# Optimization experiments

Hardware: AMD Instinct MI355X
Metric: run time of the kernel (lower is better)

## Reference

```python
import jax, jax.numpy as jnp
import numpy as np

NUM_USERS = 1024
NUM_BUSINESSES = 2048
N_NODES = NUM_USERS + NUM_BUSINESSES  # 3072
B = 1024            # batch size (== NUM_USERS to keep the business_idx-offset bug valid)
E = 16384           # edges (self loops added inside reference, PyG GATConv default)
H = 768             # hidden_size
HEADS = 8
NUM_IMAGES = 3


def setup_inputs() -> dict:
    key = jax.random.key(0)
    ks = jax.random.split(key, 24)
    def rn(k, shape, s=0.02):
        return jax.random.normal(k, shape, dtype=jnp.float32) * s
    inp = {
        'text_cls': rn(ks[0], (B, 768), 1.0),              # BERT CLS features
        'img_cls': rn(ks[1], (B, NUM_IMAGES, 768), 1.0),   # ViT CLS features per image
        'biz_feats': rn(ks[2], (B, 3), 1.0),
        'W_text': rn(ks[3], (768, H)), 'b_text': jnp.zeros((H,), jnp.float32),
        'W_img': rn(ks[4], (768, H)), 'b_img': jnp.zeros((H,), jnp.float32),
        'W_bf': rn(ks[5], (3, H)), 'b_bf': jnp.zeros((H,), jnp.float32),
        'user_table': rn(ks[6], (NUM_USERS, H)),
        'biz_table': rn(ks[7], (NUM_BUSINESSES, H)),
        'W1': rn(ks[8], (H, HEADS * H)),
        'att_src1': rn(ks[9], (HEADS, H), 0.1),
        'att_dst1': rn(ks[10], (HEADS, H), 0.1),
        'b1': jnp.zeros((HEADS * H,), jnp.float32),
        'W2': rn(ks[11], (HEADS * H, H)),
        'att_src2': rn(ks[12], (1, H), 0.1),
        'att_dst2': rn(ks[13], (1, H), 0.1),
        'b2': jnp.zeros((H,), jnp.float32),
        'Wf1': rn(ks[14], (4 * H, 2 * H)), 'bf1': jnp.zeros((2 * H,), jnp.float32),
        'Wf2': rn(ks[15], (2 * H, H)), 'bf2': jnp.zeros((H,), jnp.float32),
        'Wf3': rn(ks[16], (H, 1)), 'bf3': jnp.zeros((1,), jnp.float32),
        'user_idx': jax.random.randint(ks[17], (B,), 0, NUM_USERS),
        'business_idx': jax.random.randint(ks[18], (B,), NUM_USERS, N_NODES),
        'edge_index': jax.random.randint(ks[19], (2, E), 0, N_NODES),
    }
    return inp


def gat_conv(x, src, dst, W, a_src, a_dst, bias, heads):
    # PyG GATConv: linear -> per-head additive attention -> scatter softmax over dst -> scatter add
    N = x.shape[0]
    C = W.shape[1] // heads
    h = (x @ W).reshape(N, heads, C)                       # [N,H,C]
    s_src = jnp.sum(h * a_src, axis=-1)                    # [N,H]
    s_dst = jnp.sum(h * a_dst, axis=-1)                    # [N,H]
    e = jax.nn.leaky_relu(s_src[src] + s_dst[dst], 0.2)    # [E,H]
    e_max = jax.ops.segment_max(e, dst, num_segments=N)    # [N,H]
    ee = jnp.exp(e - e_max[dst])
    denom = jax.ops.segment_sum(ee, dst, num_segments=N)   # [N,H]
    alpha = ee / (denom[dst] + 1e-16)                      # [E,H]
    out = jax.ops.segment_sum(h[src] * alpha[..., None], dst, num_segments=N)  # [N,H,C]
    return out.reshape(N, heads * C) + bias


def reference(text_cls, img_cls, biz_feats, W_text, b_text, W_img, b_img, W_bf, b_bf,
              user_table, biz_table, W1, att_src1, att_dst1, b1, W2, att_src2, att_dst2, b2,
              Wf1, bf1, Wf2, bf2, Wf3, bf3, user_idx, business_idx, edge_index):
    text_emb = text_cls @ W_text + b_text                       # TextEncoder.fc
    img_emb = jnp.mean(img_cls, axis=1) @ W_img + b_img         # ImageEncoder mean + fc
    meta = biz_feats @ W_bf + b_bf                              # business_feature_fc
    user_emb = user_table[user_idx]
    biz_emb = biz_table[business_idx - user_idx.shape[0]]       # faithful: offset by batch size
    x = jnp.zeros((N_NODES, H), jnp.float32)
    x = x.at[user_idx].set(user_emb)
    x = x.at[business_idx].set((text_emb + img_emb + meta + biz_emb) / 4.0)
    loop = jnp.arange(N_NODES)
    src = jnp.concatenate([edge_index[0], loop])                # add self loops (PyG default)
    dst = jnp.concatenate([edge_index[1], loop])
    x = jax.nn.relu(gat_conv(x, src, dst, W1, att_src1, att_dst1, b1, HEADS))
    x = gat_conv(x, src, dst, W2, att_src2, att_dst2, b2, 1)
    cat = jnp.concatenate([x[user_idx], x[business_idx], text_emb, img_emb], axis=1)  # [B,4H]
    h1 = jax.nn.relu(cat @ Wf1 + bf1)
    h2 = jax.nn.relu(h1 @ Wf2 + bf2)
    return (h2 @ Wf3 + bf3).squeeze(-1)                         # [B]
```

## Files before the change

kernel.cpp:

```cpp
#include <hip/hip_runtime.h>
#include <hip/hip_bf16.h>

namespace {

constexpr int kB = 1024;
constexpr int kNU = 1024;
constexpr int kNB = 2048;
constexpr int kNN = 3072;
constexpr int kE = 16384;
constexpr int kET = kE + kNN;
constexpr int kH = 768;
constexpr int kHeads = 8;
constexpr int kS2 = 8;

typedef __attribute__((ext_vector_type(8))) short bf16x8_t;
typedef __attribute__((ext_vector_type(4))) float f32x4_t;

__device__ __forceinline__ float tof(float x) { return x; }
__device__ __forceinline__ float tof(__hip_bfloat16 x) { return __bfloat162float(x); }
__device__ __forceinline__ void stor(float* p, float v) { *p = v; }
__device__ __forceinline__ void stor(__hip_bfloat16* p, float v) { *p = __float2bfloat16(v); }

__device__ __forceinline__ float blo(unsigned u) {
  union { unsigned u; float f; } c; c.u = u << 16; return c.f;
}
__device__ __forceinline__ float bhi(unsigned u) {
  union { unsigned u; float f; } c; c.u = u & 0xffff0000u; return c.f;
}

__device__ __forceinline__ unsigned pk2(float a, float b) {
  union { __hip_bfloat16 h[2]; unsigned u; } c;
  c.h[0] = __float2bfloat16(a); c.h[1] = __float2bfloat16(b);
  return c.u;
}

__device__ __forceinline__ void gload_lds16(const void* g, void* l) {
  __builtin_amdgcn_global_load_lds(
      (const __attribute__((address_space(1))) void*)g,
      (__attribute__((address_space(3))) void*)l, 16, 0, 0);
}

template <int G>
__device__ __forceinline__ void wait_stage(bool more) {
  if (more) {
    if constexpr (G == 2) asm volatile("s_waitcnt vmcnt(2)" ::: "memory");
    else if constexpr (G == 3) asm volatile("s_waitcnt vmcnt(3)" ::: "memory");
    else asm volatile("s_waitcnt vmcnt(4)" ::: "memory");
  } else {
    asm volatile("s_waitcnt vmcnt(0)" ::: "memory");
  }
  __builtin_amdgcn_sched_barrier(0);
  asm volatile("s_barrier" ::: "memory");
  __builtin_amdgcn_sched_barrier(0);
}

template <int BM, int BN, int FM, int FN, typename TC>
__device__ __forceinline__ void gemm_body(
    const __hip_bfloat16* __restrict__ A, const __hip_bfloat16* __restrict__ Bt,
    const float* __restrict__ bias, TC* __restrict__ C,
    int K, int lda, int ldc, int act, int bx, int by) {
  __shared__ __align__(16) __hip_bfloat16 As[3][BM][32];
  __shared__ __align__(16) __hip_bfloat16 Bs[3][BN][32];
  constexpr int G = BM / 64 + BN / 64;
  const int t = threadIdx.x;
  const int w = t >> 6, lane = t & 63;
  const int wm = w >> 1, wn = w & 1;
  const int bm = by * BM, bn = bx * BN;
  const int lr = lane & 15, lg = lane >> 4;

  f32x4_t acc[FM][FN];
#pragma unroll
  for (int m = 0; m < FM; ++m)
#pragma unroll
    for (int n = 0; n < FN; ++n) acc[m][n] = (f32x4_t){0.f, 0.f, 0.f, 0.f};

  auto stage = [&](int buf, int kt) {
    const int k0 = kt << 5;
#pragma unroll
    for (int i = 0; i < BM / 64; ++i) {
      int L = i * 256 + t;
      gload_lds16(A + (size_t)(bm + (L >> 2)) * lda + k0 + (L & 3) * 8,
                  (char*)(&As[buf][0][0]) + ((size_t)(i * 256 + w * 64)) * 16);
    }
#pragma unroll
    for (int i = 0; i < BN / 64; ++i) {
      int L = i * 256 + t;
      gload_lds16(Bt + (size_t)(bn + (L >> 2)) * K + k0 + (L & 3) * 8,
                  (char*)(&Bs[buf][0][0]) + ((size_t)(i * 256 + w * 64)) * 16);
    }
  };

  const int NT = K >> 5;
  stage(0, 0);
  if (NT > 1) stage(1, 1);
  int cur = 0;
  for (int kt = 0; kt < NT; ++kt) {
    wait_stage<G>(kt + 1 < NT);
    if (kt + 2 < NT) {
      int sb = cur + 2; if (sb >= 3) sb -= 3;
      stage(sb, kt + 2);
    }
    bf16x8_t af[FM], bv[FN];
#pragma unroll
    for (int m = 0; m < FM; ++m)
      af[m] = *(const bf16x8_t*)&As[cur][wm * FM * 16 + m * 16 + lr][lg * 8];
#pragma unroll
    for (int n = 0; n < FN; ++n)
      bv[n] = *(const bf16x8_t*)&Bs[cur][wn * FN * 16 + n * 16 + lr][lg * 8];
#pragma unroll
    for (int m = 0; m < FM; ++m)
#pragma unroll
      for (int n = 0; n < FN; ++n)
        acc[m][n] = __builtin_amdgcn_mfma_f32_16x16x32_bf16(af[m], bv[n], acc[m][n], 0, 0, 0);
    cur = (cur == 2) ? 0 : cur + 1;
  }

#pragma unroll
  for (int m = 0; m < FM; ++m) {
    const int row0 = bm + wm * FM * 16 + m * 16 + lg * 4;
#pragma unroll
    for (int n = 0; n < FN; ++n) {
      const int cn = bn + wn * FN * 16 + n * 16 + lr;
      const float bvv = bias ? bias[cn] : 0.f;
#pragma unroll
      for (int r = 0; r < 4; ++r) {
        float v = acc[m][n][r] + bvv;
        if (act) v = fmaxf(v, 0.f);
        stor(&C[(size_t)(row0 + r) * ldc + cn], v);
      }
    }
  }
}

__device__ __forceinline__ void swz_xy(bool mfast, int& bx, int& by) {
  const int nwg = gridDim.x * gridDim.y;
  const int orig = blockIdx.y * gridDim.x + blockIdx.x;
  const int swz = (orig & 7) * (nwg >> 3) + (orig >> 3);
  if (mfast) { by = swz % gridDim.y; bx = swz / gridDim.y; }
  else       { bx = swz % gridDim.x; by = swz / gridDim.x; }
}

template <int BM, int BN, int FM, int FN>
__global__ __launch_bounds__(256) void mfma_gemm_dual(
    const __hip_bfloat16* __restrict__ A0, const __hip_bfloat16* __restrict__ Bt0,
    const float* __restrict__ bias0, float* __restrict__ C0,
    const __hip_bfloat16* __restrict__ A1, const __hip_bfloat16* __restrict__ Bt1,
    const float* __restrict__ bias1, float* __restrict__ C1,
    int N, int K) {
  int bx, by;
  swz_xy(true, bx, by);
  const __hip_bfloat16* A = blockIdx.z ? A1 : A0;
  const __hip_bfloat16* Bt = blockIdx.z ? Bt1 : Bt0;
  const float* bias = blockIdx.z ? bias1 : bias0;
  float* C = blockIdx.z ? C1 : C0;
  gemm_body<BM, BN, FM, FN, float>(A, Bt, bias, C, K, K, N, 0, bx, by);
}

template <int BM, int BN, int FM, int FN>
__global__ __launch_bounds__(256) void gemm_head(
    const __hip_bfloat16* __restrict__ y, const __hip_bfloat16* __restrict__ W1t,
    const float* __restrict__ b1, __hip_bfloat16* __restrict__ x2) {
  const int hd = blockIdx.x;
  const int tile = blockIdx.y;
  const int bx = tile % (kH / BN);
  const int by = tile / (kH / BN);
  gemm_body<BM, BN, FM, FN, __hip_bfloat16>(
      y + (size_t)hd * kH, W1t + (size_t)hd * kH * kH, b1 + hd * kH,
      x2 + (size_t)hd * kH, kH, kHeads * kH, kHeads * kH, 1, bx, by);
}

template <int BM, int BN, int FM, int FN, int S>
__global__ __launch_bounds__(256) void mfma_gemm_kpin(
    const __hip_bfloat16* __restrict__ A, const __hip_bfloat16* __restrict__ Bt,
    float* __restrict__ Cpart, int M, int N, int K) {
  __shared__ __align__(16) __hip_bfloat16 As[3][BM][32];
  __shared__ __align__(16) __hip_bfloat16 Bs[3][BN][32];
  constexpr int G = BM / 64 + BN / 64;
  const int kc = blockIdx.x;
  const int tile = blockIdx.y;
  const int tilesN = N / BN;
  const int bx = tile % tilesN;
  const int by = tile / tilesN;
  const int KC = K / S;
  const int kbeg = kc * KC;
  const int t = threadIdx.x;
  const int w = t >> 6, lane = t & 63;
  const int wm = w >> 1, wn = w & 1;
  const int bm = by * BM, bn = bx * BN;
  const int lr = lane & 15, lg = lane >> 4;

  f32x4_t acc[FM][FN];
#pragma unroll
  for (int m = 0; m < FM; ++m)
#pragma unroll
    for (int n = 0; n < FN; ++n) acc[m][n] = (f32x4_t){0.f, 0.f, 0.f, 0.f};

  auto stage = [&](int buf, int kt) {
    const int k0 = kbeg + (kt << 5);
#pragma unroll
    for (int i = 0; i < BM / 64; ++i) {
      int L = i * 256 + t;
      gload_lds16(A + (size_t)(bm + (L >> 2)) * K + k0 + (L & 3) * 8,
                  (char*)(&As[buf][0][0]) + ((size_t)(i * 256 + w * 64)) * 16);
    }
#pragma unroll
    for (int i = 0; i < BN / 64; ++i) {
      int L = i * 256 + t;
      gload_lds16(Bt + (size_t)(bn + (L >> 2)) * K + k0 + (L & 3) * 8,
                  (char*)(&Bs[buf][0][0]) + ((size_t)(i * 256 + w * 64)) * 16);
    }
  };

  const int NT = KC >> 5;
  stage(0, 0);
  if (NT > 1) stage(1, 1);
  int cur = 0;
  for (int kt = 0; kt < NT; ++kt) {
    wait_stage<G>(kt + 1 < NT);
    if (kt + 2 < NT) {
      int sb = cur + 2; if (sb >= 3) sb -= 3;
      stage(sb, kt + 2);
    }
    bf16x8_t af[FM], bv[FN];
#pragma unroll
    for (int m = 0; m < FM; ++m)
      af[m] = *(const bf16x8_t*)&As[cur][wm * FM * 16 + m * 16 + lr][lg * 8];
#pragma unroll
    for (int n = 0; n < FN; ++n)
      bv[n] = *(const bf16x8_t*)&Bs[cur][wn * FN * 16 + n * 16 + lr][lg * 8];
#pragma unroll
    for (int m = 0; m < FM; ++m)
#pragma unroll
      for (int n = 0; n < FN; ++n)
        acc[m][n] = __builtin_amdgcn_mfma_f32_16x16x32_bf16(af[m], bv[n], acc[m][n], 0, 0, 0);
    cur = (cur == 2) ? 0 : cur + 1;
  }

  float* Cp = Cpart + (size_t)kc * M * N;
#pragma unroll
  for (int m = 0; m < FM; ++m) {
    const int row0 = bm + wm * FM * 16 + m * 16 + lg * 4;
#pragma unroll
    for (int n = 0; n < FN; ++n) {
      const int cn = bn + wn * FN * 16 + n * 16 + lr;
#pragma unroll
      for (int r = 0; r < 4; ++r) Cp[(size_t)(row0 + r) * N + cn] = acc[m][n][r];
    }
  }
}

template <int BM, int BN, int FM, int FN>
__global__ __launch_bounds__(256) void mfma_gemm_splitk(
    const __hip_bfloat16* __restrict__ A, const __hip_bfloat16* __restrict__ Bt,
    float* __restrict__ Cpart, int M, int N, int K, int KC) {
  __shared__ __align__(16) __hip_bfloat16 As[3][BM][32];
  __shared__ __align__(16) __hip_bfloat16 Bs[3][BN][32];
  constexpr int G = BM / 64 + BN / 64;
  int bx, by;
  swz_xy(false, bx, by);
  const int t = threadIdx.x;
  const int w = t >> 6, lane = t & 63;
  const int wm = w >> 1, wn = w & 1;
  const int bm = by * BM, bn = bx * BN;
  const int kbeg = blockIdx.z * KC;
  const int lr = lane & 15, lg = lane >> 4;

  f32x4_t acc[FM][FN];
#pragma unroll
  for (int m = 0; m < FM; ++m)
#pragma unroll
    for (int n = 0; n < FN; ++n) acc[m][n] = (f32x4_t){0.f, 0.f, 0.f, 0.f};

  auto stage = [&](int buf, int kt) {
    const int k0 = kbeg + (kt << 5);
#pragma unroll
    for (int i = 0; i < BM / 64; ++i) {
      int L = i * 256 + t;
      gload_lds16(A + (size_t)(bm + (L >> 2)) * K + k0 + (L & 3) * 8,
                  (char*)(&As[buf][0][0]) + ((size_t)(i * 256 + w * 64)) * 16);
    }
#pragma unroll
    for (int i = 0; i < BN / 64; ++i) {
      int L = i * 256 + t;
      gload_lds16(Bt + (size_t)(bn + (L >> 2)) * K + k0 + (L & 3) * 8,
                  (char*)(&Bs[buf][0][0]) + ((size_t)(i * 256 + w * 64)) * 16);
    }
  };

  const int NT = KC >> 5;
  stage(0, 0);
  if (NT > 1) stage(1, 1);
  int cur = 0;
  for (int kt = 0; kt < NT; ++kt) {
    wait_stage<G>(kt + 1 < NT);
    if (kt + 2 < NT) {
      int sb = cur + 2; if (sb >= 3) sb -= 3;
      stage(sb, kt + 2);
    }
    bf16x8_t af[FM], bv[FN];
#pragma unroll
    for (int m = 0; m < FM; ++m)
      af[m] = *(const bf16x8_t*)&As[cur][wm * FM * 16 + m * 16 + lr][lg * 8];
#pragma unroll
    for (int n = 0; n < FN; ++n)
      bv[n] = *(const bf16x8_t*)&Bs[cur][wn * FN * 16 + n * 16 + lr][lg * 8];
#pragma unroll
    for (int m = 0; m < FM; ++m)
#pragma unroll
      for (int n = 0; n < FN; ++n)
        acc[m][n] = __builtin_amdgcn_mfma_f32_16x16x32_bf16(af[m], bv[n], acc[m][n], 0, 0, 0);
    cur = (cur == 2) ? 0 : cur + 1;
  }

  float* Cp = Cpart + (size_t)blockIdx.z * M * N;
#pragma unroll
  for (int m = 0; m < FM; ++m) {
    const int row0 = bm + wm * FM * 16 + m * 16 + lg * 4;
#pragma unroll
    for (int n = 0; n < FN; ++n) {
      const int cn = bn + wn * FN * 16 + n * 16 + lr;
#pragma unroll
      for (int r = 0; r < 4; ++r) Cp[(size_t)(row0 + r) * N + cn] = acc[m][n][r];
    }
  }
}

__global__ __launch_bounds__(192) void reduce_scores2_kernel(
    const float* __restrict__ part, const float* __restrict__ att_src,
    const float* __restrict__ att_dst, __hip_bfloat16* __restrict__ h2,
    float* __restrict__ s_src, float* __restrict__ s_dst) {
  __shared__ float redS[3], redD[3];
  const int row = blockIdx.x;
  const int t = threadIdx.x;
  const int c = t * 4;
  const float* p = part + (size_t)row * kH + c;
  float4 s = *(const float4*)p;
#pragma unroll
  for (int z = 1; z < kS2; ++z) {
    float4 qv = *(const float4*)(p + (size_t)z * kNN * kH);
    s.x += qv.x; s.y += qv.y; s.z += qv.z; s.w += qv.w;
  }
  __hip_bfloat16 b0 = __float2bfloat16(s.x), b1 = __float2bfloat16(s.y);
  __hip_bfloat16 b2 = __float2bfloat16(s.z), b3 = __float2bfloat16(s.w);
  __hip_bfloat16* o = h2 + (size_t)row * kH + c;
  o[0] = b0; o[1] = b1; o[2] = b2; o[3] = b3;
  float f0 = tof(b0), f1 = tof(b1), f2 = tof(b2), f3 = tof(b3);
  float ss = f0 * att_src[c] + f1 * att_src[c + 1] + f2 * att_src[c + 2] + f3 * att_src[c + 3];
  float sd = f0 * att_dst[c] + f1 * att_dst[c + 1] + f2 * att_dst[c + 2] + f3 * att_dst[c + 3];
#pragma unroll
  for (int off = 32; off; off >>= 1) { ss += __shfl_down(ss, off); sd += __shfl_down(sd, off); }
  if ((t & 63) == 0) { redS[t >> 6] = ss; redD[t >> 6] = sd; }
  __syncthreads();
  if (t == 0) {
    s_src[row] = redS[0] + redS[1] + redS[2];
    s_dst[row] = redD[0] + redD[1] + redD[2];
  }
}

__global__ void reduce_relu_kernel(const float* __restrict__ part,
                                   const float* __restrict__ bias,
                                   __hip_bfloat16* __restrict__ outb, int MN4, int N) {
  int i = blockIdx.x * 256 + threadIdx.x;
  if (i >= MN4) return;
  float4 s = ((const float4*)part)[i];
  float4 p = ((const float4*)part)[(size_t)MN4 + i];
  int c = (i * 4) % N;
  float v0 = fmaxf(s.x + p.x + bias[c], 0.f);
  float v1 = fmaxf(s.y + p.y + bias[c + 1], 0.f);
  float v2 = fmaxf(s.z + p.z + bias[c + 2], 0.f);
  float v3 = fmaxf(s.w + p.w + bias[c + 3], 0.f);
  uint2 o;
  o.x = pk2(v0, v1); o.y = pk2(v2, v3);
  *(uint2*)(outb + (size_t)i * 4) = o;
}

__global__ __launch_bounds__(192) void reduce_final_kernel(
    const float* __restrict__ part, const float* __restrict__ bias,
    const float* __restrict__ Wf3, const float* __restrict__ bf3,
    float* __restrict__ out) {
  __shared__ float red[3];
  const int row = blockIdx.x;
  const int t = threadIdx.x;
  const int c = t * 4;
  const float* p0 = part + (size_t)row * kH + c;
  const float* p1 = p0 + (size_t)kB * kH;
  float4 a = *(const float4*)p0;
  float4 b = *(const float4*)p1;
  float v0 = fmaxf(a.x + b.x + bias[c], 0.f);
  float v1 = fmaxf(a.y + b.y + bias[c + 1], 0.f);
  float v2 = fmaxf(a.z + b.z + bias[c + 2], 0.f);
  float v3 = fmaxf(a.w + b.w + bias[c + 3], 0.f);
  float s = v0 * Wf3[c] + v1 * Wf3[c + 1] + v2 * Wf3[c + 2] + v3 * Wf3[c + 3];
#pragma unroll
  for (int off = 32; off; off >>= 1) s += __shfl_down(s, off);
  if ((t & 63) == 0) red[t >> 6] = s;
  __syncthreads();
  if (t == 0) out[row] = red[0] + red[1] + red[2] + bf3[0];
}

struct TJobs {
  const float* in[6];
  __hip_bfloat16* out[6];
  int K[6];
  int N[6];
  int start[7];
};

__global__ __launch_bounds__(256) void transp_prep_kernel(
    TJobs j, const float* __restrict__ text_cls, const float* __restrict__ img_cls,
    __hip_bfloat16* __restrict__ text_bf, __hip_bfloat16* __restrict__ imgm_bf,
    int prep_blocks, const float* __restrict__ W1, const float* __restrict__ a_src,
    const float* __restrict__ a_dst, float* __restrict__ wa,
    int wa_blocks, uint4* __restrict__ xb4) {
  __shared__ float tl[32][33];
  const int bid = blockIdx.x;
  const int t = threadIdx.x;
  if (bid >= j.start[6] + prep_blocks + wa_blocks) {
    int i = (bid - j.start[6] - prep_blocks - wa_blocks) * 256 + t;
    if (i < kNN * kH * 2 / 16) xb4[i] = (uint4){0u, 0u, 0u, 0u};
    return;
  }
  if (bid >= j.start[6] + prep_blocks) {
    int gw = ((bid - j.start[6] - prep_blocks) * 256 + t) >> 6;
    int lane = t & 63;
    if (gw >= kHeads * kH) return;
    int i = gw >> 3, hd = gw & 7;
    const float* wrow = W1 + (size_t)i * (kHeads * kH) + hd * kH;
    const float* as = a_src + (size_t)hd * kH;
    const float* ad = a_dst + (size_t)hd * kH;
    float ss = 0.f, sd = 0.f;
    for (int c = lane; c < kH; c += 64) {
      float wv = wrow[c];
      ss = fmaf(wv, as[c], ss);
      sd = fmaf(wv, ad[c], sd);
    }
#pragma unroll
    for (int o = 32; o; o >>= 1) { ss += __shfl_down(ss, o); sd += __shfl_down(sd, o); }
    if (lane == 0) {
      wa[hd * kH + i] = ss;
      wa[kHeads * kH + hd * kH + i] = sd;
    }
    return;
  }
  if (bid >= j.start[6]) {
    int idx = (bid - j.start[6]) * 256 + t;
    if (idx < kB * kH) {
      text_bf[idx] = __float2bfloat16(text_cls[idx]);
      int b = idx / kH, c = idx - b * kH;
      const float* p = img_cls + (size_t)b * 3 * kH + c;
      imgm_bf[idx] = __float2bfloat16((p[0] + p[kH] + p[2 * kH]) * (1.f / 3.f));
    }
    return;
  }
  int idx = 0;
#pragma unroll
  for (int q = 1; q < 6; ++q)
    if (bid >= j.start[q]) idx = q;
  const int tile = bid - j.start[idx];
  const int N = j.N[idx], K = j.K[idx];
  const int tilesN = N >> 5;
  const int n0 = (tile % tilesN) << 5, k0 = (tile / tilesN) << 5;
  const float* in = j.in[idx];
  __hip_bfloat16* out = j.out[idx];
  const int r = t >> 3, c = (t & 7) * 4;
#pragma unroll
  for (int i = 0; i < 4; ++i) tl[r][c + i] = in[(size_t)(k0 + r) * N + n0 + c + i];
  __syncthreads();
  __hip_bfloat16* op = out + (size_t)(n0 + r) * K + k0 + c;
#pragma unroll
  for (int i = 0; i < 4; ++i) op[i] = __float2bfloat16(tl[c + i][r]);
}

__global__ __launch_bounds__(256) void s1_kernel(const __hip_bfloat16* __restrict__ xb,
                                                 const float* __restrict__ wa,
                                                 float* __restrict__ s1s,
                                                 float* __restrict__ s1d) {
  __shared__ unsigned xrow[kH / 2];
  const int n = blockIdx.x;
  const int t = threadIdx.x;
  const unsigned* xp = (const unsigned*)(xb + (size_t)n * kH);
  if (t < 128) { xrow[t] = xp[t]; xrow[t + 128] = xp[t + 128]; xrow[t + 256] = xp[t + 256]; }
  __syncthreads();
  const int w = t >> 6, lane = t & 63;
  const float* ws0 = wa + (size_t)w * kH;
  const float* wd0 = wa + (size_t)(kHeads + w) * kH;
  const float* ws1 = wa + (size_t)(w + 4) * kH;
  const float* wd1 = wa + (size_t)(kHeads + w + 4) * kH;
  float s0 = 0.f, d0 = 0.f, s1 = 0.f, d1 = 0.f;
  for (int u = lane; u < kH / 2; u += 64) {
    unsigned v = xrow[u];
    float f0 = blo(v), f1 = bhi(v);
    int c = u * 2;
    s0 = fmaf(f0, ws0[c], fmaf(f1, ws0[c + 1], s0));
    d0 = fmaf(f0, wd0[c], fmaf(f1, wd0[c + 1], d0));
    s1 = fmaf(f0, ws1[c], fmaf(f1, ws1[c + 1], s1));
    d1 = fmaf(f0, wd1[c], fmaf(f1, wd1[c + 1], d1));
  }
#pragma unroll
  for (int o = 32; o; o >>= 1) {
    s0 += __shfl_down(s0, o); d0 += __shfl_down(d0, o);
    s1 += __shfl_down(s1, o); d1 += __shfl_down(d1, o);
  }
  if (lane == 0) {
    s1s[n * 8 + w] = s0;     s1d[n * 8 + w] = d0;
    s1s[n * 8 + w + 4] = s1; s1d[n * 8 + w + 4] = d1;
  }
}

__global__ __launch_bounds__(256) void agg1x_kernel(
    const int* __restrict__ rowptr, const int* __restrict__ cols,
    const float* __restrict__ s1s, const float* __restrict__ s1d,
    const __hip_bfloat16* __restrict__ xb, __hip_bfloat16* __restrict__ y) {
  __shared__ float mh[8], rdh[8], sdl[8];
  __shared__ float alph[128][9];
  const int n = blockIdx.x;
  const int t = threadIdx.x, w = t >> 6, lane = t & 63;
  const int beg = rowptr[n], end = rowptr[n + 1];
  if (t < 8) sdl[t] = s1d[n * 8 + t];
  __syncthreads();
#pragma unroll
  for (int p = 0; p < 2; ++p) {
    const int h = w + p * 4;
    const float sd = sdl[h];
    float m = -3.402823466e38f;
    for (int i = beg + lane; i < end; i += 64) {
      float e = s1s[(size_t)cols[i] * 8 + h] + sd;
      e = (e > 0.f) ? e : 0.2f * e;
      m = fmaxf(m, e);
    }
#pragma unroll
    for (int o = 32; o; o >>= 1) m = fmaxf(m, __shfl_xor(m, o));
    float ds = 0.f;
    for (int i = beg + lane; i < end; i += 64) {
      float e = s1s[(size_t)cols[i] * 8 + h] + sd;
      e = (e > 0.f) ? e : 0.2f * e;
      ds += expf(e - m);
    }
#pragma unroll
    for (int o = 32; o; o >>= 1) ds += __shfl_xor(ds, o);
    if (lane == 0) { mh[h] = m; rdh[h] = 1.f / (ds + 1e-16f); }
  }
  __syncthreads();

  float acc[8][4];
#pragma unroll
  for (int h = 0; h < 8; ++h)
#pragma unroll
    for (int q = 0; q < 4; ++q) acc[h][q] = 0.f;
  const int c0 = t * 4;

  for (int chunk = beg; chunk < end; chunk += 128) {
    const int cnt = min(128, end - chunk);
#pragma unroll
    for (int p = 0; p < 2; ++p) {
      const int h = w + p * 4;
      const float sd = sdl[h], m = mh[h], rd = rdh[h];
      for (int i = lane; i < cnt; i += 64) {
        float e = s1s[(size_t)cols[chunk + i] * 8 + h] + sd;
        e = (e > 0.f) ? e : 0.2f * e;
        alph[i][h] = expf(e - m) * rd;
      }
    }
    __syncthreads();
    if (t < 192) {
      for (int i = 0; i < cnt; ++i) {
        int src = cols[chunk + i];
        uint2 v = *(const uint2*)(xb + (size_t)src * kH + c0);
        float f0 = blo(v.x), f1 = bhi(v.x), f2 = blo(v.y), f3 = bhi(v.y);
#pragma unroll
        for (int h = 0; h < 8; ++h) {
          float a = alph[i][h];
          acc[h][0] = fmaf(a, f0, acc[h][0]);
          acc[h][1] = fmaf(a, f1, acc[h][1]);
          acc[h][2] = fmaf(a, f2, acc[h][2]);
          acc[h][3] = fmaf(a, f3, acc[h][3]);
        }
      }
    }
    __syncthreads();
  }
  if (t < 192) {
#pragma unroll
    for (int h = 0; h < 8; ++h) {
      uint2 o;
      o.x = pk2(acc[h][0], acc[h][1]);
      o.y = pk2(acc[h][2], acc[h][3]);
      *(uint2*)(y + ((size_t)n * 8 + h) * kH + c0) = o;
    }
  }
}

__global__ __launch_bounds__(1024) void scan_kernel(const int* __restrict__ ei,
                                                    int* __restrict__ rowptr,
                                                    int* __restrict__ cursor) {
  __shared__ int sdeg[kNN];
  __shared__ int sums[1024];
  int t = threadIdx.x;
#pragma unroll
  for (int i = 0; i < 3; ++i) sdeg[t * 3 + i] = 0;
  __syncthreads();
  for (int e = t; e < kET; e += 1024) {
    int dst = (e < kE) ? ei[kE + e] : (e - kE);
    atomicAdd(&sdeg[dst], 1);
  }
  __syncthreads();
  int v0 = sdeg[t * 3], v1 = sdeg[t * 3 + 1], v2 = sdeg[t * 3 + 2];
  int s = v0 + v1 + v2;
  sums[t] = s;
  __syncthreads();
  for (int o = 1; o < 1024; o <<= 1) {
    int xv = (t >= o) ? sums[t - o] : 0;
    __syncthreads();
    sums[t] += xv;
    __syncthreads();
  }
  int excl = sums[t] - s;
  rowptr[t * 3] = excl;          cursor[t * 3] = excl;
  rowptr[t * 3 + 1] = excl + v0; cursor[t * 3 + 1] = excl + v0;
  rowptr[t * 3 + 2] = excl + v0 + v1; cursor[t * 3 + 2] = excl + v0 + v1;
  if (t == 1023) rowptr[kNN] = excl + s;
}

constexpr int kFillBlocks = (kET + 255) / 256;

__global__ __launch_bounds__(256) void fill_build_kernel(
    const int* __restrict__ ei, int* __restrict__ cursor, int* __restrict__ cols,
    const int* __restrict__ user_idx, const float* __restrict__ user_table,
    const int* __restrict__ business_idx, const float* __restrict__ text_emb,
    const float* __restrict__ img_emb, const float* __restrict__ biz_feats,
    const float* __restrict__ W_bf, const float* __restrict__ b_bf,
    const float* __restrict__ biz_table, __hip_bfloat16* __restrict__ xb) {
  const int bid = blockIdx.x;
  if (bid < kFillBlocks) {
    int e = bid * 256 + threadIdx.x;
    if (e >= kET) return;
    int src, dst;
    if (e < kE) { src = ei[e]; dst = ei[kE + e]; } else { src = dst = e - kE; }
    int pos = atomicAdd(&cursor[dst], 1);
    cols[pos] = src;
    return;
  }
  const int b = bid - kFillBlocks;
  if (b < kNU) {
    int node = user_idx[b];
    for (int c = threadIdx.x; c < kH; c += 256)
      xb[(size_t)node * kH + c] = __float2bfloat16(user_table[(size_t)node * kH + c]);
  } else {
    const int m = b - kNU;
    int cand = -1;
    for (int i = threadIdx.x; i < kB; i += 256)
      if (business_idx[i] == kNU + m) cand = i;
#pragma unroll
    for (int o = 32; o; o >>= 1) cand = max(cand, __shfl_xor(cand, o));
    __shared__ int red[4];
    if ((threadIdx.x & 63) == 0) red[threadIdx.x >> 6] = cand;
    __syncthreads();
    const int w = max(max(red[0], red[1]), max(red[2], red[3]));
    if (w < 0) return;
    int node = kNU + m;
    float f0 = biz_feats[w * 3], f1 = biz_feats[w * 3 + 1], f2 = biz_feats[w * 3 + 2];
    for (int c = threadIdx.x; c < kH; c += 256) {
      float meta = f0 * W_bf[c] + f1 * W_bf[kH + c] + f2 * W_bf[2 * kH + c] + b_bf[c];
      float v = (text_emb[(size_t)w * kH + c] + img_emb[(size_t)w * kH + c] + meta +
                 biz_table[(size_t)m * kH + c]) * 0.25f;
      xb[(size_t)node * kH + c] = __float2bfloat16(v);
    }
  }
}

__global__ __launch_bounds__(256) void gat_agg_kernel(
    const int* __restrict__ rowptr, const int* __restrict__ cols,
    const float* __restrict__ s_src, const float* __restrict__ s_dst,
    const __hip_bfloat16* __restrict__ h, const float* __restrict__ bias,
    float* __restrict__ out_f, int total) {
  const int pair = blockIdx.x * 4 + (threadIdx.x >> 6);
  if (pair >= total) return;
  const int lane = threadIdx.x & 63;
  const int n = pair;
  const int beg = rowptr[n], end = rowptr[n + 1];
  const float sdv = s_dst[pair];

  float m = -3.402823466e38f;
  for (int i = beg + lane; i < end; i += 64) {
    float e = s_src[cols[i]] + sdv;
    e = (e > 0.f) ? e : 0.2f * e;
    m = fmaxf(m, e);
  }
#pragma unroll
  for (int o = 32; o; o >>= 1) m = fmaxf(m, __shfl_xor(m, o));

  float dsum = 0.f;
  for (int i = beg + lane; i < end; i += 64) {
    float e = s_src[cols[i]] + sdv;
    e = (e > 0.f) ? e : 0.2f * e;
    dsum += expf(e - m);
  }
#pragma unroll
  for (int o = 32; o; o >>= 1) dsum += __shfl_xor(dsum, o);
  const float rdsum = 1.f / (dsum + 1e-16f);

  float a[12];
#pragma unroll
  for (int q = 0; q < 12; ++q) a[q] = 0.f;
  const size_t hoff = (size_t)lane * 4;
  for (int i = beg; i < end; ++i) {
    int src = cols[i];
    float e = s_src[src] + sdv;
    e = (e > 0.f) ? e : 0.2f * e;
    float wgt = expf(e - m) * rdsum;
    const __hip_bfloat16* hp = h + (size_t)src * kH + hoff;
#pragma unroll
    for (int j = 0; j < 3; ++j) {
      uint2 v = *(const uint2*)(hp + j * 256);
      a[j * 4 + 0] = fmaf(wgt, blo(v.x), a[j * 4 + 0]);
      a[j * 4 + 1] = fmaf(wgt, bhi(v.x), a[j * 4 + 1]);
      a[j * 4 + 2] = fmaf(wgt, blo(v.y), a[j * 4 + 2]);
      a[j * 4 + 3] = fmaf(wgt, bhi(v.y), a[j * 4 + 3]);
    }
  }
  const size_t ob = (size_t)n * kH + hoff;
#pragma unroll
  for (int j = 0; j < 3; ++j) {
#pragma unroll
    for (int q = 0; q < 4; ++q)
      out_f[ob + j * 256 + q] = a[j * 4 + q] + bias[hoff + j * 256 + q];
  }
}

__global__ void cat_kernel(const float* __restrict__ xf, const float* __restrict__ text_emb,
                           const float* __restrict__ img_emb, const int* __restrict__ user_idx,
                           const int* __restrict__ business_idx, __hip_bfloat16* __restrict__ cat) {
  int b = blockIdx.x;
  int u = user_idx[b], z = business_idx[b];
  __hip_bfloat16* crow = cat + (size_t)b * 4 * kH;
  for (int c = threadIdx.x; c < kH; c += blockDim.x) {
    crow[c] = __float2bfloat16(xf[(size_t)u * kH + c]);
    crow[kH + c] = __float2bfloat16(xf[(size_t)z * kH + c]);
    crow[2 * kH + c] = __float2bfloat16(text_emb[(size_t)b * kH + c]);
    crow[3 * kH + c] = __float2bfloat16(img_emb[(size_t)b * kH + c]);
  }
}

}

extern "C" void kernel_launch(void* const* d_in, const int* in_sizes, int n_in,
                              void* d_out, int out_size, void* d_ws, size_t ws_size,
                              hipStream_t stream) {
  const float* text_cls = (const float*)d_in[0];
  const float* img_cls = (const float*)d_in[1];
  const float* biz_feats = (const float*)d_in[2];
  const float* W_text = (const float*)d_in[3];
  const float* b_text = (const float*)d_in[4];
  const float* W_img = (const float*)d_in[5];
  const float* b_img = (const float*)d_in[6];
  const float* W_bf = (const float*)d_in[7];
  const float* b_bf = (const float*)d_in[8];
  const float* user_table = (const float*)d_in[9];
  const float* biz_table = (const float*)d_in[10];
  const float* W1 = (const float*)d_in[11];
  const float* att_src1 = (const float*)d_in[12];
  const float* att_dst1 = (const float*)d_in[13];
  const float* b1 = (const float*)d_in[14];
  const float* W2 = (const float*)d_in[15];
  const float* att_src2 = (const float*)d_in[16];
  const float* att_dst2 = (const float*)d_in[17];
  const float* b2 = (const float*)d_in[18];
  const float* Wf1 = (const float*)d_in[19];
  const float* bf1 = (const float*)d_in[20];
  const float* Wf2 = (const float*)d_in[21];
  const float* bf2 = (const float*)d_in[22];
  const float* Wf3 = (const float*)d_in[23];
  const float* bf3 = (const float*)d_in[24];
  const int* user_idx = (const int*)d_in[25];
  const int* business_idx = (const int*)d_in[26];
  const int* edge_index = (const int*)d_in[27];
  float* out = (float*)d_out;
  (void)in_sizes; (void)n_in; (void)out_size; (void)ws_size;

  char* base = (char*)d_ws;
  size_t off = 0;
  auto alloc = [&](size_t bytes) -> void* {
    void* p = base + off;
    off = (off + bytes + 255) & ~(size_t)255;
    return p;
  };
  __hip_bfloat16* xb = (__hip_bfloat16*)alloc((size_t)kNN * kH * 2);
  __hip_bfloat16* text_bf = (__hip_bfloat16*)alloc((size_t)kB * kH * 2);
  __hip_bfloat16* imgm_bf = (__hip_bfloat16*)alloc((size_t)kB * kH * 2);
  float* text_emb = (float*)alloc((size_t)kB * kH * 4);
  float* img_emb = (float*)alloc((size_t)kB * kH * 4);
  __hip_bfloat16* Wtt = (__hip_bfloat16*)alloc((size_t)kH * kH * 2);
  __hip_bfloat16* Wit = (__hip_bfloat16*)alloc((size_t)kH * kH * 2);
  __hip_bfloat16* W1t = (__hip_bfloat16*)alloc((size_t)kHeads * kH * kH * 2);
  __hip_bfloat16* W2t = (__hip_bfloat16*)alloc((size_t)kH * kHeads * kH * 2);
  __hip_bfloat16* Wf1t = (__hip_bfloat16*)alloc((size_t)2 * kH * 4 * kH * 2);
  __hip_bfloat16* Wf2t = (__hip_bfloat16*)alloc((size_t)kH * 2 * kH * 2);
  float* wa = (float*)alloc((size_t)2 * kHeads * kH * 4);
  __hip_bfloat16* y = (__hip_bfloat16*)alloc((size_t)kNN * kHeads * kH * 2);
  char* ext = (char*)alloc((size_t)kNN * kHeads * kH * 2);
  float* part = (float*)y;
  float* xf = (float*)ext;
  __hip_bfloat16* catb = (__hip_bfloat16*)(ext + 9437184);
  __hip_bfloat16* m1 = (__hip_bfloat16*)(ext + 9437184 + 6291456);
  __hip_bfloat16* x2 = (__hip_bfloat16*)alloc((size_t)kNN * kHeads * kH * 2);
  __hip_bfloat16* h2 = (__hip_bfloat16*)alloc((size_t)kNN * kH * 2);
  float* s1s = (float*)alloc((size_t)kNN * kHeads * 4);
  float* s1d = (float*)alloc((size_t)kNN * kHeads * 4);
  float* s2s = (float*)alloc((size_t)kNN * 4);
  float* s2d = (float*)alloc((size_t)kNN * 4);
  int* rowptr = (int*)alloc((size_t)(kNN + 1) * 4);
  int* cursor = (int*)alloc((size_t)kNN * 4);
  int* cols = (int*)alloc((size_t)kET * 4);

  TJobs tj;
  tj.in[0] = W_text; tj.out[0] = Wtt;  tj.K[0] = kH;          tj.N[0] = kH;
  tj.in[1] = W_img;  tj.out[1] = Wit;  tj.K[1] = kH;          tj.N[1] = kH;
  tj.in[2] = W1;     tj.out[2] = W1t;  tj.K[2] = kH;          tj.N[2] = kHeads * kH;
  tj.in[3] = W2;     tj.out[3] = W2t;  tj.K[3] = kHeads * kH; tj.N[3] = kH;
  tj.in[4] = Wf1;    tj.out[4] = Wf1t; tj.K[4] = 4 * kH;      tj.N[4] = 2 * kH;
  tj.in[5] = Wf2;    tj.out[5] = Wf2t; tj.K[5] = 2 * kH;      tj.N[5] = kH;
  tj.start[0] = 0;
  for (int q = 0; q < 6; ++q)
    tj.start[q + 1] = tj.start[q] + (tj.K[q] / 32) * (tj.N[q] / 32);
  const int prep_blocks = (kB * kH + 255) / 256;
  const int wa_blocks = (kHeads * kH) / 4;
  const int init_blocks = (kNN * kH * 2 / 16 + 255) / 256;
  transp_prep_kernel<<<tj.start[6] + prep_blocks + wa_blocks + init_blocks, 256, 0, stream>>>(
      tj, text_cls, img_cls, text_bf, imgm_bf, prep_blocks, W1, att_src1, att_dst1, wa,
      wa_blocks, (uint4*)xb);

  mfma_gemm_dual<64, 128, 2, 4><<<dim3(kH / 128, kB / 64, 2), 256, 0, stream>>>(
      text_bf, Wtt, b_text, text_emb, imgm_bf, Wit, b_img, img_emb, kH, kH);

  scan_kernel<<<1, 1024, 0, stream>>>(edge_index, rowptr, cursor);
  fill_build_kernel<<<kFillBlocks + kNN, 256, 0, stream>>>(
      edge_index, cursor, cols, user_idx, user_table, business_idx, text_emb, img_emb,
      biz_feats, W_bf, b_bf, biz_table, xb);

  s1_kernel<<<kNN, 256, 0, stream>>>(xb, wa, s1s, s1d);
  agg1x_kernel<<<kNN, 256, 0, stream>>>(rowptr, cols, s1s, s1d, xb, y);
  gemm_head<128, 128, 4, 4><<<dim3(kHeads, (kNN / 128) * (kH / 128)), 256, 0, stream>>>(
      y, W1t, b1, x2);

  mfma_gemm_kpin<128, 128, 4, 4, kS2>
      <<<dim3(kS2, (kNN / 128) * (kH / 128)), 256, 0, stream>>>(
          x2, W2t, part, kNN, kH, kHeads * kH);
  reduce_scores2_kernel<<<kNN, 192, 0, stream>>>(part, att_src2, att_dst2, h2, s2s, s2d);
  gat_agg_kernel<<<kNN / 4, 256, 0, stream>>>(rowptr, cols, s2s, s2d, h2, b2, xf, kNN);

  cat_kernel<<<kB, 256, 0, stream>>>(xf, text_emb, img_emb, user_idx, business_idx, catb);
  mfma_gemm_splitk<64, 128, 2, 4><<<dim3(2 * kH / 128, kB / 64, 2), 256, 0, stream>>>(
      catb, Wf1t, (float*)y, kB, 2 * kH, 4 * kH, 2 * kH);
  reduce_relu_kernel<<<(kB * 2 * kH / 4 + 255) / 256, 256, 0, stream>>>(
      (float*)y, bf1, m1, kB * 2 * kH / 4, 2 * kH);
  mfma_gemm_splitk<64, 128, 2, 4><<<dim3(kH / 128, kB / 64, 2), 256, 0, stream>>>(
      m1, Wf2t, (float*)y, kB, kH, 2 * kH, kH);
  reduce_final_kernel<<<kB, 192, 0, stream>>>((float*)y, bf2, Wf3, bf3, out);
}
```

Measured before the change: 280.7 us.

## Store split-K partials in bf16 and use double-buffered LDS pipeline

Replaces the three-stage async LDS pipeline, which used explicit vmcnt waits, with a simpler two-buffer scheme synchronised by __syncthreads in all GEMM kernels. The kpin split-K kernel now writes its partial sums as bf16 instead of fp32, and the reduce kernel reads bf16 partials, which halves the partial-buffer traffic. The ext scratch allocation is also shrunk. The bf16 partials lose accuracy in the split-K reduction, and the shallower pipeline may expose more load latency.

```diff
diff --git a/kernel.cpp b/kernel.cpp
--- a/kernel.cpp
+++ b/kernel.cpp
@@ -40,28 +40,13 @@
       (__attribute__((address_space(3))) void*)l, 16, 0, 0);
 }
 
-template <int G>
-__device__ __forceinline__ void wait_stage(bool more) {
-  if (more) {
-    if constexpr (G == 2) asm volatile("s_waitcnt vmcnt(2)" ::: "memory");
-    else if constexpr (G == 3) asm volatile("s_waitcnt vmcnt(3)" ::: "memory");
-    else asm volatile("s_waitcnt vmcnt(4)" ::: "memory");
-  } else {
-    asm volatile("s_waitcnt vmcnt(0)" ::: "memory");
-  }
-  __builtin_amdgcn_sched_barrier(0);
-  asm volatile("s_barrier" ::: "memory");
-  __builtin_amdgcn_sched_barrier(0);
-}
-
 template <int BM, int BN, int FM, int FN, typename TC>
 __device__ __forceinline__ void gemm_body(
     const __hip_bfloat16* __restrict__ A, const __hip_bfloat16* __restrict__ Bt,
     const float* __restrict__ bias, TC* __restrict__ C,
     int K, int lda, int ldc, int act, int bx, int by) {
-  __shared__ __align__(16) __hip_bfloat16 As[3][BM][32];
-  __shared__ __align__(16) __hip_bfloat16 Bs[3][BN][32];
-  constexpr int G = BM / 64 + BN / 64;
+  __shared__ __align__(16) __hip_bfloat16 As[2][BM][32];
+  __shared__ __align__(16) __hip_bfloat16 Bs[2][BN][32];
   const int t = threadIdx.x;
   const int w = t >> 6, lane = t & 63;
   const int wm = w >> 1, wn = w & 1;
@@ -92,14 +77,10 @@
 
   const int NT = K >> 5;
   stage(0, 0);
-  if (NT > 1) stage(1, 1);
-  int cur = 0;
+  __syncthreads();
   for (int kt = 0; kt < NT; ++kt) {
-    wait_stage<G>(kt + 1 < NT);
-    if (kt + 2 < NT) {
-      int sb = cur + 2; if (sb >= 3) sb -= 3;
-      stage(sb, kt + 2);
-    }
+    const int cur = kt & 1;
+    if (kt + 1 < NT) stage(cur ^ 1, kt + 1);
     bf16x8_t af[FM], bv[FN];
 #pragma unroll
     for (int m = 0; m < FM; ++m)
@@ -112,7 +93,7 @@
 #pragma unroll
       for (int n = 0; n < FN; ++n)
         acc[m][n] = __builtin_amdgcn_mfma_f32_16x16x32_bf16(af[m], bv[n], acc[m][n], 0, 0, 0);
-    cur = (cur == 2) ? 0 : cur + 1;
+    __syncthreads();
   }
 
 #pragma unroll
@@ -172,10 +153,9 @@
 template <int BM, int BN, int FM, int FN, int S>
 __global__ __launch_bounds__(256) void mfma_gemm_kpin(
     const __hip_bfloat16* __restrict__ A, const __hip_bfloat16* __restrict__ Bt,
-    float* __restrict__ Cpart, int M, int N, int K) {
-  __shared__ __align__(16) __hip_bfloat16 As[3][BM][32];
-  __shared__ __align__(16) __hip_bfloat16 Bs[3][BN][32];
-  constexpr int G = BM / 64 + BN / 64;
+    __hip_bfloat16* __restrict__ Cpart, int M, int N, int K) {
+  __shared__ __align__(16) __hip_bfloat16 As[2][BM][32];
+  __shared__ __align__(16) __hip_bfloat16 Bs[2][BN][32];
   const int kc = blockIdx.x;
   const int tile = blockIdx.y;
   const int tilesN = N / BN;
@@ -213,14 +193,10 @@
 
   const int NT = KC >> 5;
   stage(0, 0);
-  if (NT > 1) stage(1, 1);
-  int cur = 0;
+  __syncthreads();
   for (int kt = 0; kt < NT; ++kt) {
-    wait_stage<G>(kt + 1 < NT);
-    if (kt + 2 < NT) {
-      int sb = cur + 2; if (sb >= 3) sb -= 3;
-      stage(sb, kt + 2);
-    }
+    const int cur = kt & 1;
+    if (kt + 1 < NT) stage(cur ^ 1, kt + 1);
     bf16x8_t af[FM], bv[FN];
 #pragma unroll
     for (int m = 0; m < FM; ++m)
@@ -233,10 +209,10 @@
 #pragma unroll
       for (int n = 0; n < FN; ++n)
         acc[m][n] = __builtin_amdgcn_mfma_f32_16x16x32_bf16(af[m], bv[n], acc[m][n], 0, 0, 0);
-    cur = (cur == 2) ? 0 : cur + 1;
-  }
-
-  float* Cp = Cpart + (size_t)kc * M * N;
+    __syncthreads();
+  }
+
+  __hip_bfloat16* Cp = Cpart + (size_t)kc * M * N;
 #pragma unroll
   for (int m = 0; m < FM; ++m) {
     const int row0 = bm + wm * FM * 16 + m * 16 + lg * 4;
@@ -244,7 +220,8 @@
     for (int n = 0; n < FN; ++n) {
       const int cn = bn + wn * FN * 16 + n * 16 + lr;
 #pragma unroll
-      for (int r = 0; r < 4; ++r) Cp[(size_t)(row0 + r) * N + cn] = acc[m][n][r];
+      for (int r = 0; r < 4; ++r)
+        Cp[(size_t)(row0 + r) * N + cn] = __float2bfloat16(acc[m][n][r]);
     }
   }
 }
@@ -253,9 +230,8 @@
 __global__ __launch_bounds__(256) void mfma_gemm_splitk(
     const __hip_bfloat16* __restrict__ A, const __hip_bfloat16* __restrict__ Bt,
     float* __restrict__ Cpart, int M, int N, int K, int KC) {
-  __shared__ __align__(16) __hip_bfloat16 As[3][BM][32];
-  __shared__ __align__(16) __hip_bfloat16 Bs[3][BN][32];
-  constexpr int G = BM / 64 + BN / 64;
+  __shared__ __align__(16) __hip_bfloat16 As[2][BM][32];
+  __shared__ __align__(16) __hip_bfloat16 Bs[2][BN][32];
   int bx, by;
   swz_xy(false, bx, by);
   const int t = threadIdx.x;
@@ -289,14 +265,10 @@
 
   const int NT = KC >> 5;
   stage(0, 0);
-  if (NT > 1) stage(1, 1);
-  int cur = 0;
+  __syncthreads();
   for (int kt = 0; kt < NT; ++kt) {
-    wait_stage<G>(kt + 1 < NT);
-    if (kt + 2 < NT) {
-      int sb = cur + 2; if (sb >= 3) sb -= 3;
-      stage(sb, kt + 2);
-    }
+    const int cur = kt & 1;
+    if (kt + 1 < NT) stage(cur ^ 1, kt + 1);
     bf16x8_t af[FM], bv[FN];
 #pragma unroll
     for (int m = 0; m < FM; ++m)
@@ -309,7 +281,7 @@
 #pragma unroll
       for (int n = 0; n < FN; ++n)
         acc[m][n] = __builtin_amdgcn_mfma_f32_16x16x32_bf16(af[m], bv[n], acc[m][n], 0, 0, 0);
-    cur = (cur == 2) ? 0 : cur + 1;
+    __syncthreads();
   }
 
   float* Cp = Cpart + (size_t)blockIdx.z * M * N;
@@ -326,22 +298,22 @@
 }
 
 __global__ __launch_bounds__(192) void reduce_scores2_kernel(
-    const float* __restrict__ part, const float* __restrict__ att_src,
+    const __hip_bfloat16* __restrict__ part, const float* __restrict__ att_src,
     const float* __restrict__ att_dst, __hip_bfloat16* __restrict__ h2,
     float* __restrict__ s_src, float* __restrict__ s_dst) {
   __shared__ float redS[3], redD[3];
   const int row = blockIdx.x;
   const int t = threadIdx.x;
   const int c = t * 4;
-  const float* p = part + (size_t)row * kH + c;
-  float4 s = *(const float4*)p;
-#pragma unroll
-  for (int z = 1; z < kS2; ++z) {
-    float4 qv = *(const float4*)(p + (size_t)z * kNN * kH);
-    s.x += qv.x; s.y += qv.y; s.z += qv.z; s.w += qv.w;
-  }
-  __hip_bfloat16 b0 = __float2bfloat16(s.x), b1 = __float2bfloat16(s.y);
-  __hip_bfloat16 b2 = __float2bfloat16(s.z), b3 = __float2bfloat16(s.w);
+  const __hip_bfloat16* p = part + (size_t)row * kH + c;
+  float a0 = 0.f, a1 = 0.f, a2 = 0.f, a3 = 0.f;
+#pragma unroll
+  for (int z = 0; z < kS2; ++z) {
+    uint2 v = *(const uint2*)(p + (size_t)z * kNN * kH);
+    a0 += blo(v.x); a1 += bhi(v.x); a2 += blo(v.y); a3 += bhi(v.y);
+  }
+  __hip_bfloat16 b0 = __float2bfloat16(a0), b1 = __float2bfloat16(a1);
+  __hip_bfloat16 b2 = __float2bfloat16(a2), b3 = __float2bfloat16(a3);
   __hip_bfloat16* o = h2 + (size_t)row * kH + c;
   o[0] = b0; o[1] = b1; o[2] = b2; o[3] = b3;
   float f0 = tof(b0), f1 = tof(b1), f2 = tof(b2), f3 = tof(b3);
@@ -797,8 +769,8 @@
   __hip_bfloat16* Wf2t = (__hip_bfloat16*)alloc((size_t)kH * 2 * kH * 2);
   float* wa = (float*)alloc((size_t)2 * kHeads * kH * 4);
   __hip_bfloat16* y = (__hip_bfloat16*)alloc((size_t)kNN * kHeads * kH * 2);
-  char* ext = (char*)alloc((size_t)kNN * kHeads * kH * 2);
-  float* part = (float*)y;
+  char* ext = (char*)alloc(9437184 + 6291456 + 3145728);
+  __hip_bfloat16* part = (__hip_bfloat16*)y;
   float* xf = (float*)ext;
   __hip_bfloat16* catb = (__hip_bfloat16*)(ext + 9437184);
   __hip_bfloat16* m1 = (__hip_bfloat16*)(ext + 9437184 + 6291456);
```

Result: faster. 255.7 us (-8.9%).
